# Optimization experiments

Measured on AMD Instinct MI355X. Metric: run time of the kernel, lower is better.

## Reference

```python
import jax, jax.numpy as jnp
import numpy as np

D_MODEL = 1024
NUM_HEADS = 16
HEAD_DIM = D_MODEL // NUM_HEADS


def setup_inputs() -> dict:
    key = jax.random.key(0)
    ks = jax.random.split(key, 11)
    B, S = 2, 2048
    scale = 1.0 / np.sqrt(D_MODEL)
    inp = {
        "q": jax.random.normal(ks[0], (B, S, D_MODEL), jnp.float32),
        "k": jax.random.normal(ks[1], (B, S, D_MODEL), jnp.float32),
        "v": jax.random.normal(ks[2], (B, S, D_MODEL), jnp.float32),
        "Wq": jax.random.normal(ks[3], (D_MODEL, D_MODEL), jnp.float32) * scale,
        "bq": jnp.zeros((D_MODEL,), jnp.float32),
        "Wk": jax.random.normal(ks[4], (D_MODEL, D_MODEL), jnp.float32) * scale,
        "bk": jnp.zeros((D_MODEL,), jnp.float32),
        "Wv": jax.random.normal(ks[5], (D_MODEL, D_MODEL), jnp.float32) * scale,
        "bv": jnp.zeros((D_MODEL,), jnp.float32),
        "Wo": jax.random.normal(ks[6], (D_MODEL, D_MODEL), jnp.float32) * scale,
        "bo": jnp.zeros((D_MODEL,), jnp.float32),
    }
    return inp


def reference(q, k, v, Wq, bq, Wk, bk, Wv, bv, Wo, bo):
    B, S, _ = q.shape
    # Linear projections (torch Linear: x @ W.T + b), split into heads -> [b,h,s,d]
    def proj(x, W, b):
        y = jnp.einsum('bsm,nm->bsn', x, W) + b
        return y.reshape(B, -1, NUM_HEADS, HEAD_DIM).transpose(0, 2, 1, 3)
    qh = proj(q, Wq, bq)
    kh = proj(k, Wk, bk)
    vh = proj(v, Wv, bv)
    # NOTE: source scales by sqrt(d_model), NOT sqrt(head_dim) -- faithful quirk
    factor = jnp.sqrt(jnp.float32(D_MODEL))
    scores = jnp.einsum('bhqd,bhkd->bhqk', qh, kh) / factor
    attn = jax.nn.softmax(scores, axis=-1)
    out = jnp.einsum('bhqk,bhkd->bhqd', attn, vh)
    out = out.transpose(0, 2, 1, 3).reshape(B, S, D_MODEL)
    # out projection; dropout=0.0 (eval) is identity
    return jnp.einsum('bsm,nm->bsn', out, Wo) + bo
```

## Files before the change

### kernel.cpp

```cpp
#include <hip/hip_runtime.h>
#include <hip/hip_bf16.h>

typedef __hip_bfloat16 bf16;
typedef short short8 __attribute__((ext_vector_type(8)));
typedef short bs4 __attribute__((ext_vector_type(4)));
typedef float f32x4 __attribute__((ext_vector_type(4)));
typedef float f32x16 __attribute__((ext_vector_type(16)));

#define MFMA_BF16(a, b, c) __builtin_amdgcn_mfma_f32_16x16x32_bf16(a, b, c, 0, 0, 0)
#define MFMA32_BF16(a, b, c) __builtin_amdgcn_mfma_f32_32x32x16_bf16(a, b, c, 0, 0, 0)

#define QSCALE 0.045084439f

__device__ __forceinline__ void async_copy16(const bf16* g, bf16* l) {
    __builtin_amdgcn_global_load_lds(
        (const __attribute__((address_space(1))) unsigned int*)(const void*)g,
        (__attribute__((address_space(3))) unsigned int*)(void*)l, 16, 0, 0);
}

__global__ __launch_bounds__(256) void convert_all(
    const float* __restrict__ q, const float* __restrict__ k, const float* __restrict__ v,
    const float* __restrict__ wq, const float* __restrict__ wk,
    const float* __restrict__ wv, const float* __restrict__ wo,
    bf16* __restrict__ qb, bf16* __restrict__ kb, bf16* __restrict__ vb,
    bf16* __restrict__ wqb, bf16* __restrict__ wkb, bf16* __restrict__ wvb,
    bf16* __restrict__ wob)
{
    int blk = blockIdx.x;
    const float* s; bf16* d; int rel;
    if      (blk < 1024) { s = q;  d = qb;  rel = blk; }
    else if (blk < 2048) { s = k;  d = kb;  rel = blk - 1024; }
    else if (blk < 3072) { s = v;  d = vb;  rel = blk - 2048; }
    else if (blk < 3328) { s = wq; d = wqb; rel = blk - 3072; }
    else if (blk < 3584) { s = wk; d = wkb; rel = blk - 3328; }
    else if (blk < 3840) { s = wv; d = wvb; rel = blk - 3584; }
    else                 { s = wo; d = wob; rel = blk - 3840; }
    size_t base = (size_t)rel * 1024 + threadIdx.x;
#pragma unroll
    for (int i = 0; i < 4; i++) {
        float4 f = ((const float4*)s)[base + i * 256];
        union { bf16 h[4]; uint2 u; } pk;
        pk.h[0] = (bf16)f.x; pk.h[1] = (bf16)f.y;
        pk.h[2] = (bf16)f.z; pk.h[3] = (bf16)f.w;
        ((uint2*)d)[base + i * 256] = pk.u;
    }
}

__global__ __launch_bounds__(256) void gemm_qkv(
    const bf16* __restrict__ qb, const bf16* __restrict__ kb, const bf16* __restrict__ vb,
    const bf16* __restrict__ wqb, const bf16* __restrict__ wkb, const bf16* __restrict__ wvb,
    const float* __restrict__ bq, const float* __restrict__ bk, const float* __restrict__ bv,
    bf16* __restrict__ Qp, bf16* __restrict__ Kp, bf16* __restrict__ Vt)
{
    __shared__ bf16 Al[128 * 64];
    __shared__ bf16 Bl[128 * 64];

    const int sel = blockIdx.y >> 3;
    const bf16* A; const bf16* W; const float* bias;
    if      (sel == 0) { A = qb; W = wqb; bias = bq; }
    else if (sel == 1) { A = kb; W = wkb; bias = bk; }
    else               { A = vb; W = wvb; bias = bv; }

    const int K = 1024, N = 1024;
    const int t = threadIdx.x;
    const int lane = t & 63, wave = t >> 6;
    const int ln = lane & 15, quad = lane >> 4;
    const int wm = wave >> 1, wn = wave & 1;
    const int m0 = blockIdx.x * 128, n0 = (blockIdx.y & 7) * 128;

    f32x4 acc[4][4];
#pragma unroll
    for (int i = 0; i < 4; i++)
#pragma unroll
        for (int j = 0; j < 4; j++) acc[i][j] = (f32x4){0.f, 0.f, 0.f, 0.f};

    const int lk = ln & 7;
    const int srow = t >> 3, sidx0 = t & 7;

    for (int k0 = 0; k0 < K; k0 += 64) {
        const bf16* Ab = A + (size_t)m0 * K + k0;
        const bf16* Wb = W + (size_t)n0 * K + k0;
#pragma unroll
        for (int p = 0; p < 4; p++) {
            int row = p * 32 + srow, idx = sidx0 ^ (row & 7);
            async_copy16(Ab + (size_t)row * K + idx * 8, &Al[(p * 256 + wave * 64) * 8]);
        }
#pragma unroll
        for (int p = 0; p < 4; p++) {
            int row = p * 32 + srow, idx = sidx0 ^ (row & 7);
            async_copy16(Wb + (size_t)row * K + idx * 8, &Bl[(p * 256 + wave * 64) * 8]);
        }
        __syncthreads();

#pragma unroll
        for (int kk = 0; kk < 2; kk++) {
            short8 af[4], bfr[4];
#pragma unroll
            for (int i = 0; i < 4; i++) {
                int r = wm * 64 + i * 16 + ln;
                af[i] = *(const short8*)&Al[r * 64 + (((kk << 2) | quad) ^ lk) * 8];
            }
#pragma unroll
            for (int j = 0; j < 4; j++) {
                int r = wn * 64 + j * 16 + ln;
                bfr[j] = *(const short8*)&Bl[r * 64 + (((kk << 2) | quad) ^ lk) * 8];
            }
#pragma unroll
            for (int i = 0; i < 4; i++)
#pragma unroll
                for (int j = 0; j < 4; j++)
                    acc[i][j] = MFMA_BF16(af[i], bfr[j], acc[i][j]);
        }
        __syncthreads();
    }

#pragma unroll
    for (int j = 0; j < 4; j++) {
        int c = n0 + wn * 64 + j * 16 + ln;
        float bv2 = bias[c];
        if (sel == 2) {
            int h = c >> 6, dd = c & 63;
#pragma unroll
            for (int i = 0; i < 4; i++) {
                int m = m0 + wm * 64 + i * 16 + quad * 4;
                int bb = m >> 11, s = m & 2047;
                union { bf16 h4[4]; uint2 u; } pk;
#pragma unroll
                for (int r = 0; r < 4; r++) pk.h4[r] = (bf16)(acc[i][j][r] + bv2);
                *(uint2*)&Vt[(((size_t)(bb * 16 + h)) * 64 + dd) * 2048 + s] = pk.u;
            }
        } else {
            bf16* out = (sel == 0) ? Qp : Kp;
            float scl = (sel == 0) ? QSCALE : 1.0f;
#pragma unroll
            for (int i = 0; i < 4; i++) {
                int rb = m0 + wm * 64 + i * 16 + quad * 4;
#pragma unroll
                for (int r = 0; r < 4; r++)
                    out[(size_t)(rb + r) * N + c] = (bf16)((acc[i][j][r] + bv2) * scl);
            }
        }
    }
}

__global__ __launch_bounds__(256) void gemm_fin(
    const bf16* __restrict__ A, const bf16* __restrict__ W,
    const float* __restrict__ bias, float* __restrict__ C)
{
    __shared__ bf16 Al[128 * 64];
    __shared__ bf16 Bl[64 * 64];

    const int K = 1024, N = 1024;
    const int t = threadIdx.x;
    const int lane = t & 63, wave = t >> 6;
    const int ln = lane & 15, quad = lane >> 4;
    const int wm = wave >> 1, wn = wave & 1;
    const int m0 = blockIdx.x * 128, n0 = blockIdx.y * 64;

    f32x4 acc[4][2];
#pragma unroll
    for (int i = 0; i < 4; i++)
#pragma unroll
        for (int j = 0; j < 2; j++) acc[i][j] = (f32x4){0.f, 0.f, 0.f, 0.f};

    const int lk = ln & 7;
    const int srow = t >> 3, sidx0 = t & 7;

    for (int k0 = 0; k0 < K; k0 += 64) {
        const bf16* Ab = A + (size_t)m0 * K + k0;
        const bf16* Wb = W + (size_t)n0 * K + k0;
#pragma unroll
        for (int p = 0; p < 4; p++) {
            int row = p * 32 + srow, idx = sidx0 ^ (row & 7);
            async_copy16(Ab + (size_t)row * K + idx * 8, &Al[(p * 256 + wave * 64) * 8]);
        }
#pragma unroll
        for (int p = 0; p < 2; p++) {
            int row = p * 32 + srow, idx = sidx0 ^ (row & 7);
            async_copy16(Wb + (size_t)row * K + idx * 8, &Bl[(p * 256 + wave * 64) * 8]);
        }
        __syncthreads();

#pragma unroll
        for (int kk = 0; kk < 2; kk++) {
            short8 af[4], bfr[2];
#pragma unroll
            for (int i = 0; i < 4; i++) {
                int r = wm * 64 + i * 16 + ln;
                af[i] = *(const short8*)&Al[r * 64 + (((kk << 2) | quad) ^ lk) * 8];
            }
#pragma unroll
            for (int j = 0; j < 2; j++) {
                int r = wn * 32 + j * 16 + ln;
                bfr[j] = *(const short8*)&Bl[r * 64 + (((kk << 2) | quad) ^ lk) * 8];
            }
#pragma unroll
            for (int i = 0; i < 4; i++)
#pragma unroll
                for (int j = 0; j < 2; j++)
                    acc[i][j] = MFMA_BF16(af[i], bfr[j], acc[i][j]);
        }
        __syncthreads();
    }

#pragma unroll
    for (int j = 0; j < 2; j++) {
        int c = n0 + wn * 32 + j * 16 + ln;
        float bv2 = bias[c];
#pragma unroll
        for (int i = 0; i < 4; i++) {
            int rb = m0 + wm * 64 + i * 16 + quad * 4;
#pragma unroll
            for (int r = 0; r < 4; r++)
                C[(size_t)(rb + r) * N + c] = acc[i][j][r] + bv2;
        }
    }
}

__global__ __launch_bounds__(512, 4) void attn128q(
    const bf16* __restrict__ Q, const bf16* __restrict__ K,
    const bf16* __restrict__ V, bf16* __restrict__ O)
{
    const int S = 2048, D = 1024;
    __shared__ bf16 Kl[2][128 * 64];
    __shared__ bf16 Vl[2][64 * 128];

    const int t = threadIdx.x, lane = t & 63, wave = t >> 6;
    const int lo = lane & 31, hi = lane >> 5;
    const int keyhalf = wave >> 2;
    const int qw = wave & 3;
    const int h = blockIdx.x & 15, b = blockIdx.x >> 4, qt = blockIdx.y;
    const size_t kqbase = (size_t)b * S * D + (size_t)h * 64;
    const size_t vbase = ((size_t)(b * 16 + h)) * 64 * 2048;

    const int q0 = qt * 128 + qw * 32;
    short8 aq[4];
    {
        const bf16* qp = Q + kqbase + (size_t)(q0 + lo) * D + hi * 8;
#pragma unroll
        for (int s = 0; s < 4; s++) aq[s] = *(const short8*)(qp + s * 16);
    }
    asm volatile("" :: "v"(aq[0]), "v"(aq[1]), "v"(aq[2]), "v"(aq[3]));

    f32x16 o0, o1;
#pragma unroll
    for (int i = 0; i < 16; i++) { o0[i] = 0.f; o1[i] = 0.f; }
    f32x4 l4 = (f32x4){0.f, 0.f, 0.f, 0.f};

    int koff[4];
#pragma unroll
    for (int s = 0; s < 4; s++)
        koff[s] = lo * 64 + (((2 * s + hi) ^ (lo & 7)) * 8);
    const int khbase = keyhalf * 64 * 64;

    const int x0 = (keyhalf * 8) ^ (lo & 15);
    const int vbl = lo * 128 + hi * 4;

    const int krow = t >> 3, kidx = t & 7;
    const int vrow = t >> 4, vidx = t & 15;

#define STAGE_KV(buf_, kt_) do {                                               \
    _Pragma("unroll")                                                          \
    for (int p = 0; p < 2; p++) {                                              \
        int row = p * 64 + krow, idx = kidx ^ (row & 7);                       \
        async_copy16(K + kqbase + (size_t)((kt_) * 128 + row) * D + idx * 8,   \
                     &Kl[buf_][(p * 512 + wave * 64) * 8]);                    \
    }                                                                          \
    _Pragma("unroll")                                                          \
    for (int p = 0; p < 2; p++) {                                              \
        int row = p * 32 + vrow, idx = vidx ^ (row & 15);                      \
        async_copy16(V + vbase + (size_t)row * 2048 + (kt_) * 128 + idx * 8,   \
                     &Vl[buf_][(p * 512 + wave * 64) * 8]);                    \
    }                                                                          \
} while (0)

    STAGE_KV(0, 0);

    for (int kt = 0; kt < S / 128; kt++) {
        const int cur = kt & 1;
        if (kt < S / 128 - 1) {
            STAGE_KV(cur ^ 1, kt + 1);
            asm volatile("s_waitcnt vmcnt(4)" ::: "memory");
        } else {
            asm volatile("s_waitcnt vmcnt(0)" ::: "memory");
        }
        __builtin_amdgcn_s_barrier();

        const bf16* Klc = Kl[cur];
        const bf16* Vlc = Vl[cur];

#pragma unroll
        for (int kg = 0; kg < 2; kg++) {
            const bf16* kb = Klc + khbase + kg * (32 * 64);
            short8 kf0 = *(const short8*)(kb + koff[0]);
            short8 kf1 = *(const short8*)(kb + koff[1]);
            short8 kf2 = *(const short8*)(kb + koff[2]);
            short8 kf3 = *(const short8*)(kb + koff[3]);

            __builtin_amdgcn_s_setprio(1);
            f32x16 acc;
#pragma unroll
            for (int i = 0; i < 16; i++) acc[i] = 0.f;
            acc = MFMA32_BF16(kf0, aq[0], acc);
            acc = MFMA32_BF16(kf1, aq[1], acc);
            acc = MFMA32_BF16(kf2, aq[2], acc);
            acc = MFMA32_BF16(kf3, aq[3], acc);
            __builtin_amdgcn_s_setprio(0);

            union { bf16 hh[8]; short8 s; } pk0, pk1;
#pragma unroll
            for (int r = 0; r < 8; r++) {
                float p = __builtin_amdgcn_exp2f(acc[r]);
                l4[r & 3] += p;
                pk0.hh[r] = (bf16)p;
            }
#pragma unroll
            for (int r = 0; r < 8; r++) {
                float p = __builtin_amdgcn_exp2f(acc[8 + r]);
                l4[r & 3] += p;
                pk1.hh[r] = (bf16)p;
            }

            __builtin_amdgcn_s_setprio(1);
#pragma unroll
            for (int db = 0; db < 2; db++) {
#pragma unroll
                for (int c = 0; c < 2; c++) {
                    const int m = kg * 4 + 2 * c;
                    union { bs4 hh[2]; short8 s; } vf;
                    vf.hh[0] = *(const bs4*)&Vlc[vbl + db * 4096 + ((x0 ^ m) * 8)];
                    vf.hh[1] = *(const bs4*)&Vlc[vbl + db * 4096 + ((x0 ^ (m + 1)) * 8)];
                    if (db == 0) o0 = MFMA32_BF16(c ? pk1.s : pk0.s, vf.s, o0);
                    else         o1 = MFMA32_BF16(c ? pk1.s : pk0.s, vf.s, o1);
                }
            }
            __builtin_amdgcn_s_setprio(0);
        }

        asm volatile("" ::: "memory");
        __builtin_amdgcn_s_barrier();
    }
#undef STAGE_KV

    float lv = (l4[0] + l4[1]) + (l4[2] + l4[3]);
    lv += __shfl_xor(lv, 32);

    float* os = (float*)&Kl[0][0];
    float* ls = (float*)&Vl[0][0];
    if (wave >= 4) {
        const int w4 = wave - 4;
#pragma unroll
        for (int i = 0; i < 16; i++) os[(w4 * 32 + i) * 64 + lane] = o0[i];
#pragma unroll
        for (int i = 0; i < 16; i++) os[(w4 * 32 + 16 + i) * 64 + lane] = o1[i];
        ls[w4 * 64 + lane] = lv;
    }
    __syncthreads();
    if (wave < 4) {
#pragma unroll
        for (int i = 0; i < 16; i++) o0[i] += os[(wave * 32 + i) * 64 + lane];
#pragma unroll
        for (int i = 0; i < 16; i++) o1[i] += os[(wave * 32 + 16 + i) * 64 + lane];
        lv += ls[wave * 64 + lane];
        float inv = __builtin_amdgcn_rcpf(lv);
#pragma unroll
        for (int r = 0; r < 16; r++) {
            const int q = (r & 3) + 8 * (r >> 2) + 4 * hi;
            float invr = __shfl(inv, q);
            const int row = qt * 128 + qw * 32 + q;
            bf16* op = O + ((size_t)b * S + row) * D + h * 64 + lo;
            op[0]  = (bf16)(o0[r] * invr);
            op[32] = (bf16)(o1[r] * invr);
        }
    }
}

extern "C" void kernel_launch(void* const* d_in, const int* in_sizes, int n_in,
                              void* d_out, int out_size, void* d_ws, size_t ws_size,
                              hipStream_t stream) {
    (void)in_sizes; (void)n_in; (void)out_size; (void)ws_size;
    const float* q  = (const float*)d_in[0];
    const float* k  = (const float*)d_in[1];
    const float* v  = (const float*)d_in[2];
    const float* Wq = (const float*)d_in[3];
    const float* bq = (const float*)d_in[4];
    const float* Wk = (const float*)d_in[5];
    const float* bk = (const float*)d_in[6];
    const float* Wv = (const float*)d_in[7];
    const float* bv = (const float*)d_in[8];
    const float* Wo = (const float*)d_in[9];
    const float* bo = (const float*)d_in[10];
    float* out = (float*)d_out;

    const int M = 4096, N = 1024;
    const size_t MN = (size_t)M * N;
    const size_t NN = (size_t)N * N;
    bf16* qb  = (bf16*)d_ws;
    bf16* kb  = qb + MN;
    bf16* vb  = kb + MN;
    bf16* wqb = vb + MN;
    bf16* wkb = wqb + NN;
    bf16* wvb = wkb + NN;
    bf16* wob = wvb + NN;
    bf16* Qp  = wob + NN;
    bf16* Kp  = Qp + MN;
    bf16* Vt  = Kp + MN;
    bf16* AO  = qb;

    dim3 blk(256);
    convert_all<<<4096, blk, 0, stream>>>(q, k, v, Wq, Wk, Wv, Wo,
                                          qb, kb, vb, wqb, wkb, wvb, wob);

    gemm_qkv<<<dim3(32, 24), blk, 0, stream>>>(qb, kb, vb, wqb, wkb, wvb,
                                               bq, bk, bv, Qp, Kp, Vt);

    attn128q<<<dim3(32, 16), dim3(512), 0, stream>>>(Qp, Kp, Vt, AO);

    gemm_fin<<<dim3(32, 16), blk, 0, stream>>>(AO, wob, bo, out);
}
```

Before: 221.5 us.

## Double-buffer output GEMM loads and enlarge tile to 128x128

The final output-projection GEMM now prefetches the next K-slice into a second LDS buffer with async global-to-LDS copies while the current slice is consumed. It uses partial vmcnt waits and raw barriers instead of full __syncthreads. The N tile also grows from 64 to 128 columns per block, which halves the grid and doubles per-wave MFMA work and B reuse. The cost is more LDS and accumulator registers, fewer blocks across the CUs, and reliance on hand-written waitcnt ordering for correctness.

```diff
diff --git a/kernel.cpp b/kernel.cpp
--- a/kernel.cpp
+++ b/kernel.cpp
@@ -147,65 +147,87 @@
     const bf16* __restrict__ A, const bf16* __restrict__ W,
     const float* __restrict__ bias, float* __restrict__ C)
 {
-    __shared__ bf16 Al[128 * 64];
-    __shared__ bf16 Bl[64 * 64];
+    __shared__ bf16 Al[2][128 * 64];
+    __shared__ bf16 Bl[2][128 * 64];
 
     const int K = 1024, N = 1024;
     const int t = threadIdx.x;
     const int lane = t & 63, wave = t >> 6;
     const int ln = lane & 15, quad = lane >> 4;
     const int wm = wave >> 1, wn = wave & 1;
-    const int m0 = blockIdx.x * 128, n0 = blockIdx.y * 64;
-
-    f32x4 acc[4][2];
+    const int m0 = blockIdx.x * 128, n0 = blockIdx.y * 128;
+
+    f32x4 acc[4][4];
 #pragma unroll
     for (int i = 0; i < 4; i++)
 #pragma unroll
-        for (int j = 0; j < 2; j++) acc[i][j] = (f32x4){0.f, 0.f, 0.f, 0.f};
+        for (int j = 0; j < 4; j++) acc[i][j] = (f32x4){0.f, 0.f, 0.f, 0.f};
 
     const int lk = ln & 7;
     const int srow = t >> 3, sidx0 = t & 7;
 
+#define STAGE_AB(buf_, k0_) do {                                               \
+    const bf16* Ab = A + (size_t)m0 * K + (k0_);                               \
+    const bf16* Wb = W + (size_t)n0 * K + (k0_);                               \
+    _Pragma("unroll")                                                          \
+    for (int p = 0; p < 4; p++) {                                              \
+        int row = p * 32 + srow, idx = sidx0 ^ (row & 7);                      \
+        async_copy16(Ab + (size_t)row * K + idx * 8,                           \
+                     &Al[buf_][(p * 256 + wave * 64) * 8]);                    \
+    }                                                                          \
+    _Pragma("unroll")                                                          \
+    for (int p = 0; p < 4; p++) {                                              \
+        int row = p * 32 + srow, idx = sidx0 ^ (row & 7);                      \
+        async_copy16(Wb + (size_t)row * K + idx * 8,                           \
+                     &Bl[buf_][(p * 256 + wave * 64) * 8]);                    \
+    }                                                                          \
+} while (0)
+
+    STAGE_AB(0, 0);
+
     for (int k0 = 0; k0 < K; k0 += 64) {
-        const bf16* Ab = A + (size_t)m0 * K + k0;
-        const bf16* Wb = W + (size_t)n0 * K + k0;
-#pragma unroll
-        for (int p = 0; p < 4; p++) {
-            int row = p * 32 + srow, idx = sidx0 ^ (row & 7);
-            async_copy16(Ab + (size_t)row * K + idx * 8, &Al[(p * 256 + wave * 64) * 8]);
-        }
-#pragma unroll
-        for (int p = 0; p < 2; p++) {
-            int row = p * 32 + srow, idx = sidx0 ^ (row & 7);
-            async_copy16(Wb + (size_t)row * K + idx * 8, &Bl[(p * 256 + wave * 64) * 8]);
-        }
-        __syncthreads();
+        const int cur = (k0 >> 6) & 1;
+        if (k0 < K - 64) {
+            STAGE_AB(cur ^ 1, k0 + 64);
+            asm volatile("s_waitcnt vmcnt(8)" ::: "memory");
+        } else {
+            asm volatile("s_waitcnt vmcnt(0)" ::: "memory");
+        }
+        __builtin_amdgcn_s_barrier();
+
+        const bf16* Alc = Al[cur];
+        const bf16* Blc = Bl[cur];
 
 #pragma unroll
         for (int kk = 0; kk < 2; kk++) {
-            short8 af[4], bfr[2];
+            short8 af[4], bfr[4];
 #pragma unroll
             for (int i = 0; i < 4; i++) {
                 int r = wm * 64 + i * 16 + ln;
-                af[i] = *(const short8*)&Al[r * 64 + (((kk << 2) | quad) ^ lk) * 8];
-            }
-#pragma unroll
-            for (int j = 0; j < 2; j++) {
-                int r = wn * 32 + j * 16 + ln;
-                bfr[j] = *(const short8*)&Bl[r * 64 + (((kk << 2) | quad) ^ lk) * 8];
-            }
+                af[i] = *(const short8*)&Alc[r * 64 + (((kk << 2) | quad) ^ lk) * 8];
+            }
+#pragma unroll
+            for (int j = 0; j < 4; j++) {
+                int r = wn * 64 + j * 16 + ln;
+                bfr[j] = *(const short8*)&Blc[r * 64 + (((kk << 2) | quad) ^ lk) * 8];
+            }
+            __builtin_amdgcn_s_setprio(1);
 #pragma unroll
             for (int i = 0; i < 4; i++)
 #pragma unroll
-                for (int j = 0; j < 2; j++)
+                for (int j = 0; j < 4; j++)
                     acc[i][j] = MFMA_BF16(af[i], bfr[j], acc[i][j]);
-        }
-        __syncthreads();
-    }
-
-#pragma unroll
-    for (int j = 0; j < 2; j++) {
-        int c = n0 + wn * 32 + j * 16 + ln;
+            __builtin_amdgcn_s_setprio(0);
+        }
+
+        asm volatile("" ::: "memory");
+        __builtin_amdgcn_s_barrier();
+    }
+#undef STAGE_AB
+
+#pragma unroll
+    for (int j = 0; j < 4; j++) {
+        int c = n0 + wn * 64 + j * 16 + ln;
         float bv2 = bias[c];
 #pragma unroll
         for (int i = 0; i < 4; i++) {
@@ -416,5 +438,5 @@
 
     attn128q<<<dim3(32, 16), dim3(512), 0, stream>>>(Qp, Kp, Vt, AO);
 
-    gemm_fin<<<dim3(32, 16), blk, 0, stream>>>(AO, wob, bo, out);
-}
+    gemm_fin<<<dim3(32, 8), blk, 0, stream>>>(AO, wob, bo, out);
+}
```

New measurement: 223.5 us. About the same (+0.9%).
